# Kernel tuning notes

Hardware: AMD Instinct MI355X
Metric: run time of the kernel (lower is better)

Reference implementation:

```python
import jax, jax.numpy as jnp
import numpy as np

BETA = 0.2  # encoder_fit_vq_factor
K = 4096    # codebook_size
D = 256     # codeword_size
B, T = 8, 2048


def setup_inputs() -> dict:
    key = jax.random.key(0)
    k1, k2 = jax.random.split(key)
    x = jax.random.normal(k1, (B, T, D), dtype=jnp.float32)
    # torch init: uniform(-1/n^2, 1/n^2) with n=1 -> uniform(-1, 1)
    embedding = jax.random.uniform(k2, (K, D), dtype=jnp.float32, minval=-1.0, maxval=1.0)
    return {"x": x, "embedding": embedding}


def reference(x, embedding):
    dist = (
        jnp.sum(x * x, axis=2, keepdims=True)
        + jnp.sum(embedding * embedding, axis=1)
        - 2.0 * jnp.einsum("btd,kd->btk", x, embedding)
    )
    indexes = jnp.argmin(dist, axis=2)  # [B, T]
    # one_hot @ embedding is just a gather (same math, no [B,T,K] one-hot)
    values = jnp.take(embedding, indexes, axis=0)  # [B, T, D]
    loss1 = jnp.mean((jax.lax.stop_gradient(x) - values) ** 2)
    loss2 = jnp.mean((x - jax.lax.stop_gradient(values)) ** 2)
    out = x + jax.lax.stop_gradient(values - x)  # straight-through estimator
    return out, indexes, loss1 + BETA * loss2
```

## Files before the change

kernel.cpp:

```cpp
#include <hip/hip_runtime.h>
#include <hip/hip_bf16.h>

#define N_ROWS 16384
#define K_CODES 4096
#define D_DIM 256

typedef short short8 __attribute__((ext_vector_type(8)));
typedef float floatx4 __attribute__((ext_vector_type(4)));

__device__ inline void gload_lds16(const void* g, void* l) {
    __builtin_amdgcn_global_load_lds(
        (const __attribute__((address_space(1))) void*)g,
        (__attribute__((address_space(3))) void*)l, 16, 0, 0);
}

__global__ __launch_bounds__(256) void vq_pack(const float* __restrict__ x,
                                               const float* __restrict__ e,
                                               uint4* __restrict__ X,
                                               uint4* __restrict__ E,
                                               float* __restrict__ xx,
                                               float* __restrict__ en) {
    int tid  = threadIdx.x;
    int w    = blockIdx.x * 4 + (tid >> 6);
    int lane = tid & 63;
    int sub  = lane >> 5, q = lane & 31;
    const float* src;
    uint4* img;
    float* ndst;
    int row;
    if (w < 8192) { row = w * 2 + sub;          src = x; img = X; ndst = xx; }
    else          { row = (w - 8192) * 2 + sub; src = e; img = E; ndst = en; }
    int rb = row >> 7, r = row & 127;
    int ch = q >> 2, ps = (q & 3) ^ (r & 3);
    uint4* dstH = img + rb * 8192 + ch * 1024 + r * 4 + ps;
    uint4* dstL = dstH + 512;

    float4 v0 = *reinterpret_cast<const float4*>(&src[(size_t)row * D_DIM + q * 8]);
    float4 v1 = *reinterpret_cast<const float4*>(&src[(size_t)row * D_DIM + q * 8 + 4]);
    float f[8] = {v0.x, v0.y, v0.z, v0.w, v1.x, v1.y, v1.z, v1.w};

    float s = 0.f;
    unsigned int hh[8], ll[8];
#pragma unroll
    for (int i = 0; i < 8; ++i) {
        s += f[i] * f[i];
        unsigned int u = __float_as_uint(f[i]);
        hh[i] = u >> 16;
        float lo = f[i] - __uint_as_float(u & 0xFFFF0000u);
        ll[i] = __float_as_uint(lo) >> 16;
    }
#pragma unroll
    for (int m = 1; m <= 16; m <<= 1) s += __shfl_xor(s, m, 64);
    if (q == 0) ndst[row] = s;

    *dstH = make_uint4(hh[0] | (hh[1] << 16), hh[2] | (hh[3] << 16),
                       hh[4] | (hh[5] << 16), hh[6] | (hh[7] << 16));
    *dstL = make_uint4(ll[0] | (ll[1] << 16), ll[2] | (ll[3] << 16),
                       ll[4] | (ll[5] << 16), ll[6] | (ll[7] << 16));
}

__global__ __launch_bounds__(256) void vq_argmin(const uint4* __restrict__ X,
                                                 const uint4* __restrict__ E,
                                                 const float* __restrict__ en,
                                                 const float* __restrict__ xx,
                                                 unsigned long long* __restrict__ top2) {
    __shared__ __align__(16) unsigned short sm[2048 * 8];

    int tid  = threadIdx.x;
    int cbk  = blockIdx.x & 31;
    int rb   = blockIdx.x >> 5;
    int r0   = rb * 128, c0 = cbk * 128;
    int lane = tid & 63;
    int wave = tid >> 6;
    int wm   = wave >> 1, wn = wave & 1;
    int l15  = lane & 15, lq = lane >> 4;

    floatx4 acc[4][4];
#pragma unroll
    for (int mt = 0; mt < 4; ++mt)
#pragma unroll
        for (int nt = 0; nt < 4; ++nt) acc[mt][nt] = (floatx4)0.f;

    const uint4* Ag = X + (size_t)rb  * 8192;
    const uint4* Bg = E + (size_t)cbk * 8192;

    const short8* Av = reinterpret_cast<const short8*>(sm);
    int sw = lq ^ (l15 & 3);
    int ua = (wm * 64 + l15) * 4 + sw;
    int ub = (wn * 64 + l15) * 4 + sw;

    for (int ch = 0; ch < 8; ++ch) {
        __syncthreads();
#pragma unroll
        for (int i = 0; i < 4; ++i) {
            int q = i * 256 + tid;
            gload_lds16(Ag + ch * 1024 + q, (char*)sm + (i * 256 + wave * 64) * 16);
            gload_lds16(Bg + ch * 1024 + q, (char*)sm + ((1024 + i * 256) + wave * 64) * 16);
        }
        __syncthreads();

        short8 ah[4], al[4];
#pragma unroll
        for (int t = 0; t < 4; ++t) {
            ah[t] = Av[ua + t * 64];
            al[t] = Av[512 + ua + t * 64];
        }
#pragma unroll
        for (int nt = 0; nt < 4; ++nt) {
            short8 bh = Av[1024 + ub + nt * 64];
            short8 bl = Av[1536 + ub + nt * 64];
#pragma unroll
            for (int mt = 0; mt < 4; ++mt) {
                acc[mt][nt] = __builtin_amdgcn_mfma_f32_16x16x32_bf16(ah[mt], bh, acc[mt][nt], 0, 0, 0);
                acc[mt][nt] = __builtin_amdgcn_mfma_f32_16x16x32_bf16(ah[mt], bl, acc[mt][nt], 0, 0, 0);
                acc[mt][nt] = __builtin_amdgcn_mfma_f32_16x16x32_bf16(al[mt], bh, acc[mt][nt], 0, 0, 0);
            }
        }
    }

    float xv[4][4], ev[4];
#pragma unroll
    for (int mt = 0; mt < 4; ++mt)
#pragma unroll
        for (int r = 0; r < 4; ++r)
            xv[mt][r] = xx[r0 + wm * 64 + mt * 16 + lq * 4 + r];
#pragma unroll
    for (int nt = 0; nt < 4; ++nt) ev[nt] = en[c0 + wn * 64 + nt * 16 + l15];

    __syncthreads();
    unsigned long long* cand = (unsigned long long*)sm;

#pragma unroll
    for (int mt = 0; mt < 4; ++mt) {
#pragma unroll
        for (int r = 0; r < 4; ++r) {
            unsigned int b0 = 0xFFFFFFFFu, b1 = 0xFFFFFFFFu;
#pragma unroll
            for (int nt = 0; nt < 4; ++nt) {
                float dist = (xv[mt][r] + ev[nt]) - 2.0f * acc[mt][nt][r];
                unsigned int u = __float_as_uint(dist);
                u ^= (u & 0x80000000u) ? 0xFFFFFFFFu : 0x80000000u;
                unsigned int key = (u & 0xFFFFF000u) |
                                   (unsigned)(c0 + wn * 64 + nt * 16 + l15);
                if (key < b0) { b1 = b0; b0 = key; }
                else if (key < b1) b1 = key;
            }
            int row_local = wm * 64 + mt * 16 + lq * 4 + r;
            cand[(row_local * 2 + wn) * 16 + l15] =
                ((unsigned long long)b0 << 32) | b1;
        }
    }
    __syncthreads();

    {
        unsigned int B0 = 0xFFFFFFFFu, B1 = 0xFFFFFFFFu;
        const unsigned long long* cb = cand + tid * 16;
#pragma unroll
        for (int j = 0; j < 8; ++j) {
            int o = ((j + tid) & 7) * 2;
            unsigned long long p0 = cb[o], p1 = cb[o + 1];
            unsigned int o0 = (unsigned int)(p0 >> 32), o1 = (unsigned int)p0;
            unsigned int mx = B0 > o0 ? B0 : o0;
            B0 = B0 < o0 ? B0 : o0;
            unsigned int mn = B1 < o1 ? B1 : o1;
            B1 = mx < mn ? mx : mn;
            o0 = (unsigned int)(p1 >> 32); o1 = (unsigned int)p1;
            mx = B0 > o0 ? B0 : o0;
            B0 = B0 < o0 ? B0 : o0;
            mn = B1 < o1 ? B1 : o1;
            B1 = mx < mn ? mx : mn;
        }
        top2[(size_t)(r0 + (tid >> 1)) * 64 + cbk * 2 + (tid & 1)] =
            ((unsigned long long)B0 << 32) | B1;
    }
}

__global__ __launch_bounds__(256) void vq_merge(const float* __restrict__ x,
                                                const float* __restrict__ e,
                                                const float* __restrict__ en,
                                                const float* __restrict__ xx,
                                                const unsigned long long* __restrict__ top2,
                                                float* __restrict__ out,
                                                double* __restrict__ partials) {
    int tid  = threadIdx.x;
    int lane = tid & 63;
    int wave = tid >> 6;
    int row  = blockIdx.x * 4 + wave;

    unsigned long long c = top2[(size_t)row * 64 + lane];
    unsigned int k0 = (unsigned int)(c >> 32);
    unsigned int k1 = (unsigned int)c;
    unsigned int k2 = 0xFFFFFFFFu, k3 = 0xFFFFFFFFu;
#pragma unroll
    for (int m = 1; m <= 32; m <<= 1) {
        unsigned int o0 = __shfl_xor(k0, m, 64);
        unsigned int o1 = __shfl_xor(k1, m, 64);
        unsigned int o2 = __shfl_xor(k2, m, 64);
        unsigned int o3 = __shfl_xor(k3, m, 64);
        unsigned int t0 = min(k0, o0), s0 = max(k0, o0);
        unsigned int t1 = min(k1, o1), s1 = max(k1, o1);
        unsigned int t2 = min(k2, o2);
        unsigned int t3 = min(k3, o3);
        k0 = t0;
        k1 = min(s0, t1);
        unsigned int u = max(s0, t1);
        k2 = min(u, t2);
        k3 = min(max(u, t2), min(s1, t3));
    }
    int i0 = k0 & 0xFFF, i1 = k1 & 0xFFF, i2 = k2 & 0xFFF, i3 = k3 & 0xFFF;

    float4 xv = reinterpret_cast<const float4*>(x)[(size_t)row * 64 + lane];
    float4 e0 = reinterpret_cast<const float4*>(e)[(size_t)i0 * 64 + lane];
    float4 e1 = reinterpret_cast<const float4*>(e)[(size_t)i1 * 64 + lane];
    float4 e2 = reinterpret_cast<const float4*>(e)[(size_t)i2 * 64 + lane];
    float4 e3 = reinterpret_cast<const float4*>(e)[(size_t)i3 * 64 + lane];
    double p0 = (double)xv.x * e0.x + (double)xv.y * e0.y + (double)xv.z * e0.z + (double)xv.w * e0.w;
    double p1 = (double)xv.x * e1.x + (double)xv.y * e1.y + (double)xv.z * e1.z + (double)xv.w * e1.w;
    double p2 = (double)xv.x * e2.x + (double)xv.y * e2.y + (double)xv.z * e2.z + (double)xv.w * e2.w;
    double p3 = (double)xv.x * e3.x + (double)xv.y * e3.y + (double)xv.z * e3.z + (double)xv.w * e3.w;
#pragma unroll
    for (int m = 32; m; m >>= 1) {
        p0 += __shfl_xor(p0, m, 64);
        p1 += __shfl_xor(p1, m, 64);
        p2 += __shfl_xor(p2, m, 64);
        p3 += __shfl_xor(p3, m, 64);
    }
    double xr = (double)xx[row];
    double d0 = (xr + (double)en[i0]) - 2.0 * p0;
    double d1 = (xr + (double)en[i1]) - 2.0 * p1;
    double d2 = (xr + (double)en[i2]) - 2.0 * p2;
    double d3 = (xr + (double)en[i3]) - 2.0 * p3;

    double bd = d0; int bi = i0; float4 v = e0;
    if (d1 < bd || (d1 == bd && i1 < bi)) { bd = d1; bi = i1; v = e1; }
    if (d2 < bd || (d2 == bd && i2 < bi)) { bd = d2; bi = i2; v = e2; }
    if (d3 < bd || (d3 == bd && i3 < bi)) { bd = d3; bi = i3; v = e3; }

    float4 o;
    o.x = xv.x + (v.x - xv.x);
    o.y = xv.y + (v.y - xv.y);
    o.z = xv.z + (v.z - xv.z);
    o.w = xv.w + (v.w - xv.w);
    reinterpret_cast<float4*>(out)[(size_t)row * 64 + lane] = o;
    if (lane == 0) out[(size_t)N_ROWS * D_DIM + row] = (float)bi;

    float sx = xv.x - v.x, sy = xv.y - v.y, sz = xv.z - v.z, sw = xv.w - v.w;
    float ls = sx * sx + sy * sy + sz * sz + sw * sw;
#pragma unroll
    for (int m = 32; m; m >>= 1) ls += __shfl_xor(ls, m, 64);
    __shared__ float lred[4];
    if (lane == 0) lred[wave] = ls;
    __syncthreads();
    if (tid == 0)
        partials[blockIdx.x] = (double)lred[0] + (double)lred[1]
                             + (double)lred[2] + (double)lred[3];
}

__global__ __launch_bounds__(256) void vq_final(const double* __restrict__ partials,
                                                float* __restrict__ out) {
    int tid = threadIdx.x;
    double s = 0.0;
#pragma unroll
    for (int i = 0; i < 16; ++i) s += partials[tid + i * 256];
#pragma unroll
    for (int m = 32; m; m >>= 1) s += __shfl_xor(s, m, 64);
    __shared__ double dred[4];
    if ((tid & 63) == 0) dred[tid >> 6] = s;
    __syncthreads();
    if (tid == 0) {
        double tot = dred[0] + dred[1] + dred[2] + dred[3];
        float L = (float)(tot / (double)((size_t)N_ROWS * D_DIM));
        out[(size_t)N_ROWS * D_DIM + N_ROWS] = L + 0.2f * L;
    }
}

extern "C" void kernel_launch(void* const* d_in, const int* in_sizes, int n_in,
                              void* d_out, int out_size, void* d_ws, size_t ws_size,
                              hipStream_t stream) {
    const float* x = (const float*)d_in[0];
    const float* e = (const float*)d_in[1];
    float* out = (float*)d_out;
    char* ws = (char*)d_ws;
    double* partials = (double*)ws;
    float* en = (float*)(ws + 32768);
    float* xx = (float*)(ws + 49152);
    unsigned long long* top2 = (unsigned long long*)(ws + 114688);
    uint4* Ximg = (uint4*)(ws + 8503296);
    uint4* Eimg = (uint4*)(ws + 25280512);

    vq_pack<<<2560, 256, 0, stream>>>(x, e, Ximg, Eimg, xx, en);
    vq_argmin<<<4096, 256, 0, stream>>>(Ximg, Eimg, en, xx, top2);
    vq_merge<<<4096, 256, 0, stream>>>(x, e, en, xx, top2, out, partials);
    vq_final<<<1, 256, 0, stream>>>(partials, out);
}
```

Before: 182.4 us.

## Split norm computation from packing and interleave hi/lo bf16 image layout

Moves the row squared-norm computation into a separate vq_prep kernel. vq_pack is reorganized so each lane writes one 16-byte chunk (either the high or the low bf16 part) with consecutive lanes writing contiguous addresses. The packed image layout changes so the hi and lo parts of a row's chunk sit next to each other, and the argmin kernel's LDS read offsets are updated to match. The goal is coalesced stores in the pack step, at the cost of an extra kernel launch and x/e being read a second time for the norms.

```diff
diff --git a/kernel.cpp b/kernel.cpp
--- a/kernel.cpp
+++ b/kernel.cpp
@@ -14,49 +14,60 @@
         (__attribute__((address_space(3))) void*)l, 16, 0, 0);
 }
 
+__global__ __launch_bounds__(256) void vq_prep(const float* __restrict__ x,
+                                               const float* __restrict__ e,
+                                               float* __restrict__ en,
+                                               float* __restrict__ xx) {
+    int tid  = threadIdx.x;
+    int w    = blockIdx.x * 4 + (tid >> 6);
+    int lane = tid & 63;
+    const float* src;
+    float* dst;
+    if (w < K_CODES) { src = e + (size_t)w * D_DIM;             dst = en + w; }
+    else             { src = x + (size_t)(w - K_CODES) * D_DIM; dst = xx + (w - K_CODES); }
+    float4 v = reinterpret_cast<const float4*>(src)[lane];
+    float s = v.x * v.x + v.y * v.y + v.z * v.z + v.w * v.w;
+#pragma unroll
+    for (int m = 32; m; m >>= 1) s += __shfl_xor(s, m, 64);
+    if (lane == 0) *dst = s;
+}
+
 __global__ __launch_bounds__(256) void vq_pack(const float* __restrict__ x,
                                                const float* __restrict__ e,
                                                uint4* __restrict__ X,
-                                               uint4* __restrict__ E,
-                                               float* __restrict__ xx,
-                                               float* __restrict__ en) {
+                                               uint4* __restrict__ E) {
     int tid  = threadIdx.x;
     int w    = blockIdx.x * 4 + (tid >> 6);
     int lane = tid & 63;
-    int sub  = lane >> 5, q = lane & 31;
+    int ri = lane >> 3, part = (lane >> 2) & 1, ps = lane & 3;
+
     const float* src;
     uint4* img;
-    float* ndst;
-    int row;
-    if (w < 8192) { row = w * 2 + sub;          src = x; img = X; ndst = xx; }
-    else          { row = (w - 8192) * 2 + sub; src = e; img = E; ndst = en; }
-    int rb = row >> 7, r = row & 127;
-    int ch = q >> 2, ps = (q & 3) ^ (r & 3);
-    uint4* dstH = img + rb * 8192 + ch * 1024 + r * 4 + ps;
-    uint4* dstL = dstH + 512;
-
-    float4 v0 = *reinterpret_cast<const float4*>(&src[(size_t)row * D_DIM + q * 8]);
-    float4 v1 = *reinterpret_cast<const float4*>(&src[(size_t)row * D_DIM + q * 8 + 4]);
+    int rg, ch;
+    if (w < 16384) { rg = w >> 3;            ch = w & 7; src = x; img = X; }
+    else           { int v = w - 16384; rg = v >> 3; ch = v & 7; src = e; img = E; }
+
+    int row = rg * 8 + ri;
+    int b   = row >> 7, rl = row & 127;
+    int d0  = ch * 32 + ((ps ^ (rl & 3)) * 8);
+
+    const float* p = src + (size_t)row * D_DIM + d0;
+    float4 v0 = reinterpret_cast<const float4*>(p)[0];
+    float4 v1 = reinterpret_cast<const float4*>(p)[1];
     float f[8] = {v0.x, v0.y, v0.z, v0.w, v1.x, v1.y, v1.z, v1.w};
-
-    float s = 0.f;
-    unsigned int hh[8], ll[8];
+    unsigned int bts[8];
 #pragma unroll
     for (int i = 0; i < 8; ++i) {
-        s += f[i] * f[i];
         unsigned int u = __float_as_uint(f[i]);
-        hh[i] = u >> 16;
-        float lo = f[i] - __uint_as_float(u & 0xFFFF0000u);
-        ll[i] = __float_as_uint(lo) >> 16;
-    }
-#pragma unroll
-    for (int m = 1; m <= 16; m <<= 1) s += __shfl_xor(s, m, 64);
-    if (q == 0) ndst[row] = s;
-
-    *dstH = make_uint4(hh[0] | (hh[1] << 16), hh[2] | (hh[3] << 16),
-                       hh[4] | (hh[5] << 16), hh[6] | (hh[7] << 16));
-    *dstL = make_uint4(ll[0] | (ll[1] << 16), ll[2] | (ll[3] << 16),
-                       ll[4] | (ll[5] << 16), ll[6] | (ll[7] << 16));
+        if (part == 0) bts[i] = u >> 16;
+        else {
+            float lo = f[i] - __uint_as_float(u & 0xFFFF0000u);
+            bts[i] = __float_as_uint(lo) >> 16;
+        }
+    }
+    img[(size_t)b * 8192 + ch * 1024 + (rg & 15) * 64 + lane] =
+        make_uint4(bts[0] | (bts[1] << 16), bts[2] | (bts[3] << 16),
+                   bts[4] | (bts[5] << 16), bts[6] | (bts[7] << 16));
 }
 
 __global__ __launch_bounds__(256) void vq_argmin(const uint4* __restrict__ X,
@@ -85,9 +96,9 @@
     const uint4* Bg = E + (size_t)cbk * 8192;
 
     const short8* Av = reinterpret_cast<const short8*>(sm);
-    int sw = lq ^ (l15 & 3);
-    int ua = (wm * 64 + l15) * 4 + sw;
-    int ub = (wn * 64 + l15) * 4 + sw;
+    int uaq = (l15 & 7) * 8 + (lq ^ (l15 & 3));
+    int A0  = (wm * 8 + (l15 >> 3)) * 64 + uaq;
+    int B0  = 1024 + (wn * 8 + (l15 >> 3)) * 64 + uaq;
 
     for (int ch = 0; ch < 8; ++ch) {
         __syncthreads();
@@ -102,13 +113,13 @@
         short8 ah[4], al[4];
 #pragma unroll
         for (int t = 0; t < 4; ++t) {
-            ah[t] = Av[ua + t * 64];
-            al[t] = Av[512 + ua + t * 64];
+            ah[t] = Av[A0 + t * 128];
+            al[t] = Av[A0 + t * 128 + 4];
         }
 #pragma unroll
         for (int nt = 0; nt < 4; ++nt) {
-            short8 bh = Av[1024 + ub + nt * 64];
-            short8 bl = Av[1536 + ub + nt * 64];
+            short8 bh = Av[B0 + nt * 128];
+            short8 bl = Av[B0 + nt * 128 + 4];
 #pragma unroll
             for (int mt = 0; mt < 4; ++mt) {
                 acc[mt][nt] = __builtin_amdgcn_mfma_f32_16x16x32_bf16(ah[mt], bh, acc[mt][nt], 0, 0, 0);
@@ -288,7 +299,8 @@
     uint4* Ximg = (uint4*)(ws + 8503296);
     uint4* Eimg = (uint4*)(ws + 25280512);
 
-    vq_pack<<<2560, 256, 0, stream>>>(x, e, Ximg, Eimg, xx, en);
+    vq_prep<<<5120, 256, 0, stream>>>(x, e, en, xx);
+    vq_pack<<<5120, 256, 0, stream>>>(x, e, Ximg, Eimg);
     vq_argmin<<<4096, 256, 0, stream>>>(Ximg, Eimg, en, xx, top2);
     vq_merge<<<4096, 256, 0, stream>>>(x, e, en, xx, top2, out, partials);
     vq_final<<<1, 256, 0, stream>>>(partials, out);
```

New measurement: 197.8 us. +8.5%, slower.
